# Kernel tuning notes

Measured on AMD Instinct MI355X. Metric: run time of the kernel, lower is better.

## Reference

```python
import jax, jax.numpy as jnp
import numpy as np

jax.config.update("jax_enable_x64", True)  # original casts to double for cov/cholesky

B, C, H, W, DR = 64, 2048, 14, 14, 256
EPS = 1e-6      # LCMCOV eps added to covariance diagonal
BN_EPS = 1e-5   # torch BatchNorm2d default eps


def setup_inputs() -> dict:
    key = jax.random.key(0)
    k0, k1 = jax.random.split(key)
    x = jax.random.normal(k0, (B, C, H, W), dtype=jnp.float32)
    # 1x1 conv weight (kaiming fan_out for relu): std = sqrt(2 / fan_out), fan_out = DR*1*1... torch uses fan_out = out_ch*k*k per output; approximate with sqrt(2/C) scale on (DR, C)
    w_conv = jax.random.normal(k1, (DR, C), dtype=jnp.float32) * np.sqrt(2.0 / C).astype(np.float32)
    gamma = jnp.ones((DR,), jnp.float32)
    beta = jnp.zeros((DR,), jnp.float32)
    run_mean = jnp.zeros((DR,), jnp.float32)
    run_var = jnp.ones((DR,), jnp.float32)
    return {"x": x, "w_conv": w_conv, "gamma": gamma, "beta": beta,
            "run_mean": run_mean, "run_var": run_var}


def reference(x, w_conv, gamma, beta, run_mean, run_var):
    b, c, h, w = x.shape
    dr = w_conv.shape[0]
    m = h * w
    # 1x1 conv (no bias) + BatchNorm2d (eval mode, running stats) + ReLU
    y = jnp.einsum('bchw,dc->bdhw', x, w_conv)
    scale = gamma / jnp.sqrt(run_var + BN_EPS)
    y = y * scale[None, :, None, None] + (beta - run_mean * scale)[None, :, None, None]
    y = jax.nn.relu(y)
    # Covpool in float64: x I_hat x^T == (1/M) * (x - mean)(x - mean)^T
    xd = y.reshape(b, dr, m).astype(jnp.float64)
    xc = xd - xd.mean(axis=2, keepdims=True)  # [B, DR, M]
    cov = jnp.einsum('bdm,bem->bde', xc, xc) / m  # [B, DR, DR]
    # LogI_LCM: Cholesky, log the diagonal, symmetrize
    cov = cov + EPS * jnp.eye(dr, dtype=jnp.float64)
    L = jnp.linalg.cholesky(cov)
    diag = jnp.log(jnp.diagonal(L, axis1=-2, axis2=-1))          # [B, DR]
    tril = jnp.tril(L, -1) + jnp.eye(dr, dtype=L.dtype) * diag[:, :, None]
    sym = tril + jnp.swapaxes(tril, -1, -2)
    # Triuvec: upper-triangular (incl diag) entries in row-major order, cast to float32
    iu, ju = jnp.triu_indices(dr)
    return sym[:, iu, ju].astype(jnp.float32)  # [B, DR*(DR+1)/2]
```

## Files before the change

### kernel.cpp

```cpp
#include <hip/hip_runtime.h>
#include <math.h>

#define BB 64
#define CC 2048
#define MM 196
#define DD 256
#define NTOT (BB * MM)

typedef __attribute__((ext_vector_type(8))) short short8;
typedef __attribute__((ext_vector_type(4))) short short4v;
typedef __attribute__((ext_vector_type(4))) unsigned short ushort4v;
typedef __attribute__((ext_vector_type(4))) float f32x4;

__device__ __forceinline__ unsigned short bf16_rne(float f) {
  unsigned int u = __float_as_uint(f);
  unsigned int r = u + 0x7FFFu + ((u >> 16) & 1u);
  return (unsigned short)(r >> 16);
}

__global__ __launch_bounds__(256) void k_prep(
    const float* __restrict__ w, const float* __restrict__ gamma,
    const float* __restrict__ beta, const float* __restrict__ rmean,
    const float* __restrict__ rvar, unsigned short* __restrict__ wh,
    unsigned short* __restrict__ wl, float* __restrict__ sclv,
    float* __restrict__ sftv) {
  const int e0 = (blockIdx.x * 256 + threadIdx.x) * 4;
  f32x4 v = *(const f32x4*)(w + e0);
  ushort4v h, l;
#pragma unroll
  for (int i = 0; i < 4; ++i) {
    unsigned short hb = bf16_rne(v[i]);
    float hf = __uint_as_float((unsigned int)hb << 16);
    h[i] = hb;
    l[i] = bf16_rne(v[i] - hf);
  }
  *(ushort4v*)(wh + e0) = h;
  *(ushort4v*)(wl + e0) = l;
  if (blockIdx.x == 0 && threadIdx.x < DD) {
    int d = threadIdx.x;
    float s = gamma[d] / sqrtf(rvar[d] + 1e-5f);
    sclv[d] = s;
    sftv[d] = beta[d] - rmean[d] * s;
  }
}

__global__ __launch_bounds__(256, 2) void k_conv(
    const float* __restrict__ x, const unsigned short* __restrict__ wh,
    const unsigned short* __restrict__ wl, const float* __restrict__ sclv,
    const float* __restrict__ sftv, float* __restrict__ yt) {
  const int tid = threadIdx.x;
  const int wid = tid >> 6, lane = tid & 63;
  const int quad = lane >> 4, l16 = lane & 15;
  const int n0 = blockIdx.x * 64;

  __shared__ unsigned short Xh[64][36];
  __shared__ unsigned short Xl[64][36];

  f32x4 acc[4][4];
#pragma unroll
  for (int i = 0; i < 4; ++i)
#pragma unroll
    for (int j = 0; j < 4; ++j) acc[i][j] = (f32x4)0.f;

  const int nX = tid & 63, kq = tid >> 6;
  const int gn = n0 + nX;
  const int bX = gn / MM, mX = gn - bX * MM;
  const float* xp = x + (size_t)bX * CC * MM + mX;

  float xr[8];
#pragma unroll
  for (int p = 0; p < 8; ++p) xr[p] = xp[(size_t)(kq * 8 + p) * MM];

  size_t aoff[4];
#pragma unroll
  for (int ds = 0; ds < 4; ++ds)
    aoff[ds] = (size_t)(wid * 64 + ds * 16 + l16) * CC + quad * 8;

  short8 Ah[4], Al[4], Ah2[4], Al2[4];
#pragma unroll
  for (int ds = 0; ds < 4; ++ds) {
    Ah[ds] = *(const short8*)(wh + aoff[ds]);
    Al[ds] = *(const short8*)(wl + aoff[ds]);
  }

  for (int c = 0; c < 64; ++c) {
    const int k0 = c * 32;
    __syncthreads();
    {
      ushort4v h0, h1, l0, l1;
#pragma unroll
      for (int p = 0; p < 4; ++p) {
        unsigned short hb = bf16_rne(xr[p]);
        float hf = __uint_as_float((unsigned int)hb << 16);
        h0[p] = hb;
        l0[p] = bf16_rne(xr[p] - hf);
      }
#pragma unroll
      for (int p = 0; p < 4; ++p) {
        unsigned short hb = bf16_rne(xr[4 + p]);
        float hf = __uint_as_float((unsigned int)hb << 16);
        h1[p] = hb;
        l1[p] = bf16_rne(xr[4 + p] - hf);
      }
      *(ushort4v*)&Xh[nX][kq * 8] = h0;
      *(ushort4v*)&Xh[nX][kq * 8 + 4] = h1;
      *(ushort4v*)&Xl[nX][kq * 8] = l0;
      *(ushort4v*)&Xl[nX][kq * 8 + 4] = l1;
    }
    __syncthreads();
    if (c < 63) {
#pragma unroll
      for (int p = 0; p < 8; ++p)
        xr[p] = xp[(size_t)(k0 + 32 + kq * 8 + p) * MM];
#pragma unroll
      for (int ds = 0; ds < 4; ++ds) {
        Ah2[ds] = *(const short8*)(wh + aoff[ds] + k0 + 32);
        Al2[ds] = *(const short8*)(wl + aoff[ds] + k0 + 32);
      }
    }
#pragma unroll
    for (int ns = 0; ns < 4; ++ns) {
      const unsigned short* bp = &Xh[ns * 16 + l16][quad * 8];
      short4v b0 = *(const short4v*)bp;
      short4v b1 = *(const short4v*)(bp + 4);
      short8 Bh = __builtin_shufflevector(b0, b1, 0, 1, 2, 3, 4, 5, 6, 7);
      const unsigned short* bq = &Xl[ns * 16 + l16][quad * 8];
      short4v c0 = *(const short4v*)bq;
      short4v c1 = *(const short4v*)(bq + 4);
      short8 Bl = __builtin_shufflevector(c0, c1, 0, 1, 2, 3, 4, 5, 6, 7);
#pragma unroll
      for (int ds = 0; ds < 4; ++ds) {
        acc[ds][ns] = __builtin_amdgcn_mfma_f32_16x16x32_bf16(
            Ah[ds], Bh, acc[ds][ns], 0, 0, 0);
        acc[ds][ns] = __builtin_amdgcn_mfma_f32_16x16x32_bf16(
            Ah[ds], Bl, acc[ds][ns], 0, 0, 0);
        acc[ds][ns] = __builtin_amdgcn_mfma_f32_16x16x32_bf16(
            Al[ds], Bh, acc[ds][ns], 0, 0, 0);
      }
    }
#pragma unroll
    for (int ds = 0; ds < 4; ++ds) {
      Ah[ds] = Ah2[ds];
      Al[ds] = Al2[ds];
    }
  }

#pragma unroll
  for (int ds = 0; ds < 4; ++ds) {
    const int dbase = wid * 64 + ds * 16 + quad * 4;
    f32x4 s4 = *(const f32x4*)(sclv + dbase);
    f32x4 f4 = *(const f32x4*)(sftv + dbase);
#pragma unroll
    for (int ns = 0; ns < 4; ++ns) {
      const int n = n0 + ns * 16 + l16;
      const int b = n / MM, m = n - b * MM;
      f32x4 o;
#pragma unroll
      for (int r = 0; r < 4; ++r) {
        float v = fmaf(acc[ds][ns][r], s4[r], f4[r]);
        o[r] = v > 0.f ? v : 0.f;
      }
      *(f32x4*)(yt + ((size_t)b * MM + m) * DD + dbase) = o;
    }
  }
}

__global__ __launch_bounds__(256) void k_means(const float* __restrict__ yt,
                                               double* __restrict__ mean) {
  const int b = blockIdx.x;
  const int d = threadIdx.x;
  const float* p = yt + (size_t)b * MM * DD + d;
  double s0 = 0, s1 = 0, s2 = 0, s3 = 0;
  for (int m = 0; m < MM; m += 4) {
    s0 += (double)p[(size_t)(m + 0) * DD];
    s1 += (double)p[(size_t)(m + 1) * DD];
    s2 += (double)p[(size_t)(m + 2) * DD];
    s3 += (double)p[(size_t)(m + 3) * DD];
  }
  mean[b * DD + d] = (s0 + s1 + s2 + s3) * (1.0 / MM);
}

__global__ __launch_bounds__(256) void k_cov(const float* __restrict__ yt,
                                             const double* __restrict__ mean,
                                             double* __restrict__ cov) {
  const int b = blockIdx.x;
  const int t = blockIdx.y;
  const int ti = (t < 1) ? 0 : (t < 3) ? 1 : (t < 6) ? 2 : 3;
  const int tj = t - (ti * (ti + 1)) / 2;
  const int i0 = ti * 64, j0 = tj * 64;
  const int tid = threadIdx.x;
  const int tx = tid & 15, ty = tid >> 4;

  __shared__ double As[32][66];
  __shared__ double Bs[32][66];

  double acc[4][4];
#pragma unroll
  for (int i = 0; i < 4; ++i)
#pragma unroll
    for (int j = 0; j < 4; ++j) acc[i][j] = 0.0;

  const int dl = tid & 63, kl = tid >> 6;
  const double mA = mean[b * DD + i0 + dl];
  const double mB = mean[b * DD + j0 + dl];
  const float* ybase = yt + (size_t)b * MM * DD;

  for (int k0 = 0; k0 < MM; k0 += 32) {
    __syncthreads();
#pragma unroll
    for (int p = 0; p < 8; ++p) {
      int k = kl + p * 4;
      int m = k0 + k;
      double av = 0.0, bv = 0.0;
      if (m < MM) {
        av = (double)ybase[(size_t)m * DD + i0 + dl] - mA;
        bv = (double)ybase[(size_t)m * DD + j0 + dl] - mB;
      }
      As[k][dl] = av;
      Bs[k][dl] = bv;
    }
    __syncthreads();
#pragma unroll
    for (int k = 0; k < 32; ++k) {
      double a[4], bv[4];
#pragma unroll
      for (int i = 0; i < 4; ++i) a[i] = As[k][ty * 4 + i];
#pragma unroll
      for (int j = 0; j < 4; ++j) bv[j] = Bs[k][tx * 4 + j];
#pragma unroll
      for (int i = 0; i < 4; ++i)
#pragma unroll
        for (int j = 0; j < 4; ++j) acc[i][j] = fma(a[i], bv[j], acc[i][j]);
    }
  }

  double* cb = cov + (size_t)b * DD * DD;
#pragma unroll
  for (int i = 0; i < 4; ++i) {
#pragma unroll
    for (int j = 0; j < 4; ++j) {
      int gi = i0 + ty * 4 + i, gj = j0 + tx * 4 + j;
      double v = acc[i][j] * (1.0 / MM);
      if (gi == gj) v += 1e-6;
      cb[(size_t)gi * DD + gj] = v;
      if (ti != tj) cb[(size_t)gj * DD + gi] = v;
    }
  }
}

__global__ __launch_bounds__(256) void k_panel2(double* __restrict__ cov,
                                                int kb) {
  const int b = blockIdx.x;
  double* A = cov + (size_t)b * DD * DD;
  const int j0 = kb * 32;
  const int tid = threadIdx.x;

  __shared__ double Sp[256][33];
  __shared__ double Lp[224][33];
  __shared__ double L11s[32][33];
  __shared__ double rpivs[32];

  if (blockIdx.y == 0) {
    const int R = DD - j0;
    const int pj = j0 - 32;

    for (int e = tid; e < R * 32; e += 256) {
      int r = e >> 5, c = e & 31;
      Sp[r][c] = A[(size_t)(j0 + r) * DD + j0 + c];
      if (kb > 0) Lp[r][c] = A[(size_t)(j0 + r) * DD + pj + c];
    }
    __syncthreads();

    if (kb > 0) {
      const int cg = tid & 7;
      const int rg = tid >> 3;
      const int c0 = cg * 4;
      for (int r = rg; r < R; r += 32) {
        double a0 = 0, a1 = 0, a2 = 0, a3 = 0;
#pragma unroll
        for (int p = 0; p < 32; ++p) {
          double lr = Lp[r][p];
          a0 = fma(lr, Lp[c0 + 0][p], a0);
          a1 = fma(lr, Lp[c0 + 1][p], a1);
          a2 = fma(lr, Lp[c0 + 2][p], a2);
          a3 = fma(lr, Lp[c0 + 3][p], a3);
        }
        Sp[r][c0 + 0] -= a0;
        Sp[r][c0 + 1] -= a1;
        Sp[r][c0 + 2] -= a2;
        Sp[r][c0 + 3] -= a3;
      }
    }
    __syncthreads();

    if (tid < 32) {
      double r[32];
#pragma unroll
      for (int k = 0; k < 32; ++k) r[k] = Sp[tid][k];
      double rpkeep = 0.0;
#pragma unroll
      for (int j = 0; j < 32; ++j) {
        double dj = __shfl(r[j], j);
        double piv = sqrt(dj);
        double rp = 1.0 / piv;
        if (tid == j) {
          r[j] = piv;
          rpkeep = rp;
        } else {
          r[j] = r[j] * rp;
        }
        double lij = r[j];
#pragma unroll
        for (int k = j + 1; k < 32; ++k) {
          double ck = __shfl(lij, k);
          r[k] -= lij * ck;
        }
      }
#pragma unroll
      for (int k = 0; k < 32; ++k) L11s[tid][k] = (k <= tid) ? r[k] : 0.0;
      rpivs[tid] = rpkeep;
      for (int k = 0; k <= tid; ++k)
        A[(size_t)(j0 + tid) * DD + j0 + k] = r[k];
    }
    __syncthreads();

    const int T = R - 32;
    if (tid < T) {
      double q[32];
#pragma unroll
      for (int k = 0; k < 32; ++k) q[k] = Sp[32 + tid][k];
#pragma unroll
      for (int j = 0; j < 32; ++j) {
        double s = q[j];
#pragma unroll
        for (int k = 0; k < 32; ++k)
          if (k < j) s -= q[k] * L11s[j][k];
        q[j] = s * rpivs[j];
      }
      double* dst = &A[(size_t)(j0 + 32 + tid) * DD + j0];
#pragma unroll
      for (int k = 0; k < 32; ++k) dst[k] = q[k];
    }
  } else {
    const int o = j0 + 32;
    const int S = DD - o;
    const int pj = j0 - 32;
    int tI = 0, tJ = (int)blockIdx.y - 1;
    while (tJ > tI) {
      tJ -= (tI + 1);
      tI++;
    }
    const int i0 = tI * 64, jj0 = tJ * 64;
    const int txl = tid & 15, tyl = tid >> 4;

    double(*Ea)[33] = (double(*)[33])(&Lp[0][0]);
    double(*Eb)[33] = (double(*)[33])(&Lp[64][0]);

    for (int e = tid; e < 64 * 32; e += 256) {
      int r = e >> 5, c = e & 31;
      Ea[r][c] = (i0 + r < S) ? A[(size_t)(o + i0 + r) * DD + pj + c] : 0.0;
      Eb[r][c] = (jj0 + r < S) ? A[(size_t)(o + jj0 + r) * DD + pj + c] : 0.0;
    }
    __syncthreads();

    double s[4][4];
#pragma unroll
    for (int i = 0; i < 4; ++i)
#pragma unroll
      for (int j = 0; j < 4; ++j) s[i][j] = 0.0;

    const int bi = tyl * 4, bj = txl * 4;
#pragma unroll
    for (int k = 0; k < 32; ++k) {
      double a[4], bv[4];
#pragma unroll
      for (int i = 0; i < 4; ++i) a[i] = Ea[bi + i][k];
#pragma unroll
      for (int j = 0; j < 4; ++j) bv[j] = Eb[bj + j][k];
#pragma unroll
      for (int i = 0; i < 4; ++i)
#pragma unroll
        for (int j = 0; j < 4; ++j) s[i][j] = fma(a[i], bv[j], s[i][j]);
    }

#pragma unroll
    for (int i = 0; i < 4; ++i)
#pragma unroll
      for (int j = 0; j < 4; ++j) {
        int gi = i0 + bi + i, gj = jj0 + bj + j;
        if (gi < S && gj < S && gi >= gj)
          A[(size_t)(o + gi) * DD + (o + gj)] -= s[i][j];
      }
  }
}

__global__ __launch_bounds__(256) void k_out(const double* __restrict__ cov,
                                             float* __restrict__ out) {
  const int b = blockIdx.y;
  int t = blockIdx.x;
  int ti = 0, tj = t;
  while (tj >= 4 - ti) {
    tj -= (4 - ti);
    ti++;
  }
  tj += ti;
  const int tid = threadIdx.x;
  const double* A = cov + (size_t)b * DD * DD;

  __shared__ float S[64][65];
  for (int e = tid; e < 4096; e += 256) {
    int jj = e >> 6, ii = e & 63;
    S[jj][ii] = (float)A[(size_t)(tj * 64 + jj) * DD + ti * 64 + ii];
  }
  __syncthreads();

  for (int e = tid; e < 4096; e += 256) {
    int ii = e >> 6, jj = e & 63;
    int i = ti * 64 + ii, j = tj * 64 + jj;
    if (j < i) continue;
    float v = S[jj][ii];
    if (i == j) v = 2.0f * logf(v);
    int off = i * DD - (i * (i - 1)) / 2 + (j - i);
    out[(size_t)b * 32896 + off] = v;
  }
}

extern "C" void kernel_launch(void* const* d_in, const int* in_sizes, int n_in,
                              void* d_out, int out_size, void* d_ws,
                              size_t ws_size, hipStream_t stream) {
  const float* x = (const float*)d_in[0];
  const float* w = (const float*)d_in[1];
  const float* gamma = (const float*)d_in[2];
  const float* beta = (const float*)d_in[3];
  const float* rmean = (const float*)d_in[4];
  const float* rvar = (const float*)d_in[5];
  float* out = (float*)d_out;

  char* ws = (char*)d_ws;
  float* yt = (float*)ws;
  double* mean = (double*)(ws + 12845056);
  double* cov = (double*)(ws + 12845056 + 131072);
  unsigned short* wh = (unsigned short*)cov;
  unsigned short* wl = wh + (DD * CC);
  float* sclv = (float*)(wl + (DD * CC));
  float* sftv = sclv + DD;

  k_prep<<<512, 256, 0, stream>>>(w, gamma, beta, rmean, rvar, wh, wl, sclv,
                                  sftv);
  k_conv<<<NTOT / 64, 256, 0, stream>>>(x, wh, wl, sclv, sftv, yt);
  k_means<<<BB, 256, 0, stream>>>(yt, mean);
  k_cov<<<dim3(BB, 10), 256, 0, stream>>>(yt, mean, cov);
  for (int kb = 0; kb < 8; ++kb) {
    int ntiles = 0;
    if (kb > 0) {
      int S = DD - (kb * 32 + 32);
      if (S > 0) {
        int nt = (S + 63) / 64;
        ntiles = nt * (nt + 1) / 2;
      }
    }
    k_panel2<<<dim3(BB, 1 + ntiles), 256, 0, stream>>>(cov, kb);
  }
  k_out<<<dim3(10, BB), 256, 0, stream>>>(cov, out);
}
```

Before: 627.9 us.

## Fuse blocked Cholesky into one left-looking kernel per batch with double-buffered panels

Replaces the eight right-looking panel/trailing-update launches with one kernel per batch matrix. Each 32-column panel is updated left-looking from all previous columns, streamed in 16-column chunks through double-buffered shared memory. Half the threads load the next chunk while the other half run the FMA update, and the result is then factored and triangular-solved as before. This removes repeated launches and the global read-modify-write of trailing tiles. In exchange, parallelism drops to 64 blocks with half the threads idle during compute, and the kernel needs a large shared-memory footprint.

Result: slower. 849.1 us (+35.2%).

```diff
diff --git a/kernel.cpp b/kernel.cpp
--- a/kernel.cpp
+++ b/kernel.cpp
@@ -248,55 +248,91 @@
   }
 }
 
-__global__ __launch_bounds__(256) void k_panel2(double* __restrict__ cov,
-                                                int kb) {
+__global__ __launch_bounds__(256) void k_chol(double* __restrict__ cov) {
   const int b = blockIdx.x;
   double* A = cov + (size_t)b * DD * DD;
-  const int j0 = kb * 32;
   const int tid = threadIdx.x;
 
-  __shared__ double Sp[256][33];
-  __shared__ double Lp[224][33];
+  __shared__ double Lh[2][224][17];
+  __shared__ double Sp[224][33];
   __shared__ double L11s[32][33];
   __shared__ double rpivs[32];
 
-  if (blockIdx.y == 0) {
+  for (int kb = 0; kb < 8; ++kb) {
+    const int j0 = kb * 32;
     const int R = DD - j0;
-    const int pj = j0 - 32;
-
-    for (int e = tid; e < R * 32; e += 256) {
-      int r = e >> 5, c = e & 31;
-      Sp[r][c] = A[(size_t)(j0 + r) * DD + j0 + c];
-      if (kb > 0) Lp[r][c] = A[(size_t)(j0 + r) * DD + pj + c];
-    }
-    __syncthreads();
 
     if (kb > 0) {
-      const int cg = tid & 7;
-      const int rg = tid >> 3;
-      const int c0 = cg * 4;
-      for (int r = rg; r < R; r += 32) {
-        double a0 = 0, a1 = 0, a2 = 0, a3 = 0;
-#pragma unroll
-        for (int p = 0; p < 32; ++p) {
-          double lr = Lp[r][p];
-          a0 = fma(lr, Lp[c0 + 0][p], a0);
-          a1 = fma(lr, Lp[c0 + 1][p], a1);
-          a2 = fma(lr, Lp[c0 + 2][p], a2);
-          a3 = fma(lr, Lp[c0 + 3][p], a3);
+      for (int e = tid; e < R * 32; e += 256) {
+        int r = e >> 5, c = e & 31;
+        Sp[r][c] = A[(size_t)(j0 + r) * DD + j0 + c];
+      }
+      for (int e = tid; e < R * 16; e += 256) {
+        int r = e >> 4, p = e & 15;
+        Lh[0][r][p] = A[(size_t)(j0 + r) * DD + p];
+      }
+      __syncthreads();
+
+      const int rg = tid >> 2, cg = tid & 3;
+      const int ni = R >> 5;
+      const int nch = kb * 2;
+      double s[7][8];
+#pragma unroll
+      for (int i = 0; i < 7; ++i)
+#pragma unroll
+        for (int j = 0; j < 8; ++j) s[i][j] = 0.0;
+
+      for (int kc = 0; kc < nch; ++kc) {
+        const int cur = kc & 1;
+        if (tid >= 128) {
+          if (kc + 1 < nch) {
+            const int koff = (kc + 1) * 16;
+            for (int e = tid - 128; e < R * 16; e += 128) {
+              int r = e >> 4, p = e & 15;
+              Lh[cur ^ 1][r][p] = A[(size_t)(j0 + r) * DD + koff + p];
+            }
+          }
+        } else {
+#pragma unroll 4
+          for (int p = 0; p < 16; ++p) {
+            double bv[8];
+#pragma unroll
+            for (int j = 0; j < 8; ++j) bv[j] = Lh[cur][8 * cg + j][p];
+#pragma unroll
+            for (int i = 0; i < 7; ++i) {
+              if (i < ni) {
+                double av = Lh[cur][rg + 32 * i][p];
+#pragma unroll
+                for (int j = 0; j < 8; ++j)
+                  s[i][j] = fma(av, bv[j], s[i][j]);
+              }
+            }
+          }
         }
-        Sp[r][c0 + 0] -= a0;
-        Sp[r][c0 + 1] -= a1;
-        Sp[r][c0 + 2] -= a2;
-        Sp[r][c0 + 3] -= a3;
-      }
-    }
-    __syncthreads();
+        __syncthreads();
+      }
+      if (tid < 128) {
+#pragma unroll
+        for (int i = 0; i < 7; ++i) {
+          if (i < ni) {
+#pragma unroll
+            for (int j = 0; j < 8; ++j)
+              Sp[rg + 32 * i][8 * cg + j] -= s[i][j];
+          }
+        }
+      }
+      __syncthreads();
+    }
 
     if (tid < 32) {
       double r[32];
-#pragma unroll
-      for (int k = 0; k < 32; ++k) r[k] = Sp[tid][k];
+      if (kb > 0) {
+#pragma unroll
+        for (int k = 0; k < 32; ++k) r[k] = Sp[tid][k];
+      } else {
+#pragma unroll
+        for (int k = 0; k < 32; ++k) r[k] = A[(size_t)(j0 + tid) * DD + j0 + k];
+      }
       double rpkeep = 0.0;
 #pragma unroll
       for (int j = 0; j < 32; ++j) {
@@ -327,70 +363,27 @@
     const int T = R - 32;
     if (tid < T) {
       double q[32];
-#pragma unroll
-      for (int k = 0; k < 32; ++k) q[k] = Sp[32 + tid][k];
+      if (kb > 0) {
+#pragma unroll
+        for (int k = 0; k < 32; ++k) q[k] = Sp[32 + tid][k];
+      } else {
+#pragma unroll
+        for (int k = 0; k < 32; ++k)
+          q[k] = A[(size_t)(j0 + 32 + tid) * DD + j0 + k];
+      }
 #pragma unroll
       for (int j = 0; j < 32; ++j) {
-        double s = q[j];
+        double sj = q[j];
 #pragma unroll
         for (int k = 0; k < 32; ++k)
-          if (k < j) s -= q[k] * L11s[j][k];
-        q[j] = s * rpivs[j];
+          if (k < j) sj -= q[k] * L11s[j][k];
+        q[j] = sj * rpivs[j];
       }
       double* dst = &A[(size_t)(j0 + 32 + tid) * DD + j0];
 #pragma unroll
       for (int k = 0; k < 32; ++k) dst[k] = q[k];
     }
-  } else {
-    const int o = j0 + 32;
-    const int S = DD - o;
-    const int pj = j0 - 32;
-    int tI = 0, tJ = (int)blockIdx.y - 1;
-    while (tJ > tI) {
-      tJ -= (tI + 1);
-      tI++;
-    }
-    const int i0 = tI * 64, jj0 = tJ * 64;
-    const int txl = tid & 15, tyl = tid >> 4;
-
-    double(*Ea)[33] = (double(*)[33])(&Lp[0][0]);
-    double(*Eb)[33] = (double(*)[33])(&Lp[64][0]);
-
-    for (int e = tid; e < 64 * 32; e += 256) {
-      int r = e >> 5, c = e & 31;
-      Ea[r][c] = (i0 + r < S) ? A[(size_t)(o + i0 + r) * DD + pj + c] : 0.0;
-      Eb[r][c] = (jj0 + r < S) ? A[(size_t)(o + jj0 + r) * DD + pj + c] : 0.0;
-    }
-    __syncthreads();
-
-    double s[4][4];
-#pragma unroll
-    for (int i = 0; i < 4; ++i)
-#pragma unroll
-      for (int j = 0; j < 4; ++j) s[i][j] = 0.0;
-
-    const int bi = tyl * 4, bj = txl * 4;
-#pragma unroll
-    for (int k = 0; k < 32; ++k) {
-      double a[4], bv[4];
-#pragma unroll
-      for (int i = 0; i < 4; ++i) a[i] = Ea[bi + i][k];
-#pragma unroll
-      for (int j = 0; j < 4; ++j) bv[j] = Eb[bj + j][k];
-#pragma unroll
-      for (int i = 0; i < 4; ++i)
-#pragma unroll
-        for (int j = 0; j < 4; ++j) s[i][j] = fma(a[i], bv[j], s[i][j]);
-    }
-
-#pragma unroll
-    for (int i = 0; i < 4; ++i)
-#pragma unroll
-      for (int j = 0; j < 4; ++j) {
-        int gi = i0 + bi + i, gj = jj0 + bj + j;
-        if (gi < S && gj < S && gi >= gj)
-          A[(size_t)(o + gi) * DD + (o + gj)] -= s[i][j];
-      }
+    __syncthreads();
   }
 }
 
@@ -450,16 +443,6 @@
   k_conv<<<NTOT / 64, 256, 0, stream>>>(x, wh, wl, sclv, sftv, yt);
   k_means<<<BB, 256, 0, stream>>>(yt, mean);
   k_cov<<<dim3(BB, 10), 256, 0, stream>>>(yt, mean, cov);
-  for (int kb = 0; kb < 8; ++kb) {
-    int ntiles = 0;
-    if (kb > 0) {
-      int S = DD - (kb * 32 + 32);
-      if (S > 0) {
-        int nt = (S + 63) / 64;
-        ntiles = nt * (nt + 1) / 2;
-      }
-    }
-    k_panel2<<<dim3(BB, 1 + ntiles), 256, 0, stream>>>(cov, kb);
-  }
+  k_chol<<<BB, 256, 0, stream>>>(cov);
   k_out<<<dim3(10, BB), 256, 0, stream>>>(cov, out);
 }
```
